# Performance work log

Measured on AMD Instinct MI355X. Metric: run time of the kernel, lower is better.

The kernel has to match this reference:

```python
import jax, jax.numpy as jnp
import numpy as np

B = 1024      # batch
M = 4096      # num_meas
W = 2         # width_per_meas
L = 2         # num_hidden_layers
Z = 64        # num_vae_latent
H = M * W     # hidden_dim = 8192


def setup_inputs() -> dict:
    key = jax.random.key(0)
    ks = jax.random.split(key, 24)

    def nrm(i, shape, scale=0.02):
        return (jax.random.normal(ks[i], shape, dtype=jnp.float32) * scale)

    return {
        "x": jax.random.normal(ks[0], (B, M), dtype=jnp.float32),
        "eps": jax.random.normal(ks[1], (B, Z), dtype=jnp.float32),
        # encoder (dense)
        "enc1_w": nrm(2, (M, M)), "enc1_b": nrm(3, (M,)),
        "enc2_w": nrm(4, (M, M)), "enc2_b": nrm(5, (M,)),
        "mu_w": nrm(6, (Z, M)), "mu_b": nrm(7, (Z,)),
        "lv_w": nrm(8, (Z, M)), "lv_b": nrm(9, (Z,)),
        # decoder mean branch: fulcon dense, hidden/output in block form
        "mean_ful_w": nrm(10, (H, Z)), "mean_ful_b": nrm(11, (H,)),
        "mean_h_w": nrm(12, (L, M, W, W)), "mean_h_b": nrm(13, (L, H)),
        "mean_out_w": nrm(14, (M, W)), "mean_out_b": nrm(15, (M,)),
        # decoder logcov branch
        "cov_ful_w": nrm(16, (H, Z)), "cov_ful_b": nrm(17, (H,)),
        "cov_h_w": nrm(18, (L, M, W, W)), "cov_h_b": nrm(19, (L, H)),
        "cov_out_w": nrm(20, (M, W)), "cov_out_b": nrm(21, (M,)),
    }


def _decoder_branch(z, ful_w, ful_b, h_w, h_b, out_w, out_b):
    # fulcon: dense latent -> hidden, then sigmoid
    a = jax.nn.sigmoid(z @ ful_w.T + ful_b)            # [B, H]
    a = a.reshape(B, M, W)                             # block-diag structure
    for l in range(L):
        # grouped block-diagonal matmul == masked dense linear of the original
        a = jax.nn.sigmoid(
            jnp.einsum('bmw,mvw->bmv', a, h_w[l]) + h_b[l].reshape(M, W)
        )
    # output mask blocks are [1, W] per measurement
    return jnp.einsum('bmw,mw->bm', a, out_w) + out_b  # [B, M]


def reference(x, eps, enc1_w, enc1_b, enc2_w, enc2_b, mu_w, mu_b, lv_w, lv_b,
              mean_ful_w, mean_ful_b, mean_h_w, mean_h_b, mean_out_w, mean_out_b,
              cov_ful_w, cov_ful_b, cov_h_w, cov_h_b, cov_out_w, cov_out_b):
    # encoder
    h = jax.nn.relu(x @ enc1_w.T + enc1_b)
    h = jax.nn.relu(h @ enc2_w.T + enc2_b)
    mu = h @ mu_w.T + mu_b
    logvar = h @ lv_w.T + lv_b
    # reparameterization (training mode, eps supplied)
    z = mu + jnp.exp(0.5 * logvar) * eps
    # decoder
    x_recon = _decoder_branch(z, mean_ful_w, mean_ful_b, mean_h_w, mean_h_b,
                              mean_out_w, mean_out_b)
    logcov = _decoder_branch(z, cov_ful_w, cov_ful_b, cov_h_w, cov_h_b,
                             cov_out_w, cov_out_b)
    return (x_recon, logcov, mu, logvar)
```

## Files before the change

### kernel.cpp

```cpp
#include <hip/hip_runtime.h>
#include <hip/hip_bf16.h>
#include <stdint.h>

typedef __hip_bfloat16 bf16;
typedef __bf16 bf16x8 __attribute__((ext_vector_type(8)));
typedef float f32x4 __attribute__((ext_vector_type(4)));

#define NB 1024
#define NM 4096
#define NZ 64
#define NH 8192

__device__ __forceinline__ float bf2f(bf16 x) { return __bfloat162float(x); }
__device__ __forceinline__ bf16 f2bf(float x) { return __float2bfloat16(x); }
__device__ __forceinline__ float sigf(float x) { return 1.f / (1.f + __expf(-x)); }

__global__ __launch_bounds__(256) void cvt_f32_bf16(const float* __restrict__ src,
                                                    bf16* __restrict__ dst, int n4) {
  const int i = blockIdx.x * 256 + threadIdx.x;
  if (i >= n4) return;
  const float4 v = ((const float4*)src)[i];
  bf16 o[4] = {f2bf(v.x), f2bf(v.y), f2bf(v.z), f2bf(v.w)};
  *(short4*)&dst[i * 4] = *(short4*)o;
}

__global__ void zero_f32(float* p, int n) {
  int i = blockIdx.x * blockDim.x + threadIdx.x;
  if (i < n) p[i] = 0.f;
}

__global__ __launch_bounds__(256) void gemm_nt(const bf16* __restrict__ A,
                                               const float* __restrict__ W,
                                               const float* __restrict__ bias,
                                               bf16* __restrict__ C,
                                               int K, int N) {
  __shared__ __attribute__((aligned(16))) bf16 smA[2][128 * 64];
  __shared__ __attribute__((aligned(16))) bf16 smB[2][64 * 64];
  const int tid  = threadIdx.x;
  const int lane = tid & 63;
  const int w    = tid >> 6;
  const int wr   = w >> 1;
  const int wc   = w & 1;

  const int lid  = blockIdx.y * 8 + blockIdx.x;
  const int wgid = (lid & 7) * 64 + (lid >> 3);
  const int row0 = (wgid & 7) * 128;
  const int col0 = (wgid >> 3) * 64;

  f32x4 acc[4][2];
#pragma unroll
  for (int i = 0; i < 4; i++)
#pragma unroll
    for (int j = 0; j < 2; j++) acc[i][j] = (f32x4){0.f, 0.f, 0.f, 0.f};

  const int swr = tid >> 2;
  const int swk = (tid & 3) * 16;
  const float* wp = W + (size_t)(col0 + swr) * K + swk;
  const int swz = (swr & 7) << 3;
  const int woff0 = swr * 64 + ((swk + 0) ^ swz);
  const int woff1 = swr * 64 + ((swk + 8) ^ swz);

  auto stage_A = [&](int buf, int kk) {
#pragma unroll
    for (int q = 0; q < 4; q++) {
      const int chunk = q * 256 + w * 64 + lane;
      const int r  = chunk >> 3;
      const int ke = ((chunk & 7) ^ (r & 7)) * 8;
      __builtin_amdgcn_global_load_lds(
          (__attribute__((address_space(1))) unsigned int*)(A + (size_t)(row0 + r) * K + (kk + ke)),
          (__attribute__((address_space(3))) unsigned int*)(&smA[buf][(q * 256 + w * 64) * 8]),
          16, 0, 0);
    }
  };

  auto write_W = [&](int buf, const float4& a, const float4& b,
                     const float4& c, const float4& d) {
    bf16 t[16] = {f2bf(a.x), f2bf(a.y), f2bf(a.z), f2bf(a.w),
                  f2bf(b.x), f2bf(b.y), f2bf(b.z), f2bf(b.w),
                  f2bf(c.x), f2bf(c.y), f2bf(c.z), f2bf(c.w),
                  f2bf(d.x), f2bf(d.y), f2bf(d.z), f2bf(d.w)};
    *(bf16x8*)&smB[buf][woff0] = ((bf16x8*)t)[0];
    *(bf16x8*)&smB[buf][woff1] = ((bf16x8*)t)[1];
  };

  auto compute = [&](int buf) {
#pragma unroll
    for (int ks = 0; ks < 64; ks += 32) {
      const int kq = ks + (lane >> 4) * 8;
      bf16x8 af[4], bfr[2];
#pragma unroll
      for (int i = 0; i < 4; i++) {
        const int r = wr * 64 + i * 16 + (lane & 15);
        af[i] = *(const bf16x8*)&smA[buf][r * 64 + (kq ^ ((r & 7) << 3))];
      }
#pragma unroll
      for (int j = 0; j < 2; j++) {
        const int r = wc * 32 + j * 16 + (lane & 15);
        bfr[j] = *(const bf16x8*)&smB[buf][r * 64 + (kq ^ ((r & 7) << 3))];
      }
#pragma unroll
      for (int i = 0; i < 4; i++)
#pragma unroll
        for (int j = 0; j < 2; j++)
          acc[i][j] = __builtin_amdgcn_mfma_f32_16x16x32_bf16(af[i], bfr[j], acc[i][j], 0, 0, 0);
    }
  };

  stage_A(0, 0);
  {
    const float4 a = *(const float4*)(wp + 0);
    const float4 b = *(const float4*)(wp + 4);
    const float4 c = *(const float4*)(wp + 8);
    const float4 d = *(const float4*)(wp + 12);
    write_W(0, a, b, c, d);
  }
  __syncthreads();

  int cur = 0;
  for (int k0 = 64; k0 < K; k0 += 64) {
    stage_A(cur ^ 1, k0);
    const float4 a = *(const float4*)(wp + k0);
    const float4 b = *(const float4*)(wp + k0 + 4);
    const float4 c = *(const float4*)(wp + k0 + 8);
    const float4 d = *(const float4*)(wp + k0 + 12);
    compute(cur);
    write_W(cur ^ 1, a, b, c, d);
    __syncthreads();
    cur ^= 1;
  }
  compute(cur);

#pragma unroll
  for (int i = 0; i < 4; i++) {
#pragma unroll
    for (int j = 0; j < 2; j++) {
      const int cc = col0 + wc * 32 + j * 16 + (lane & 15);
      const float bs = bias[cc];
#pragma unroll
      for (int t = 0; t < 4; t++) {
        const int rr = row0 + wr * 64 + i * 16 + (lane >> 4) * 4 + t;
        float v = acc[i][j][t] + bs;
        v = v > 0.f ? v : 0.f;
        C[(size_t)rr * N + cc] = f2bf(v);
      }
    }
  }
}

__global__ __launch_bounds__(256) void mulv_splitk(const bf16* __restrict__ h2,
                                                   const float* __restrict__ muw,
                                                   const float* __restrict__ lvw,
                                                   float* __restrict__ zpre) {
  __shared__ float sA[32][64];
  __shared__ float sW[32][128];
  const int tid = threadIdx.x;
  const int b0 = blockIdx.x * 64;
  const int k0 = blockIdx.y * 256;
  const int tj = tid & 15;
  const int tb = tid >> 4;
  float acc[4][8];
#pragma unroll
  for (int i = 0; i < 4; i++)
#pragma unroll
    for (int j = 0; j < 8; j++) acc[i][j] = 0.f;

  const int lb = tid >> 2, lk = (tid & 3) * 8;
  const int wj = tid >> 1, wk = (tid & 1) * 16;
  const float* wrow = (wj < 64) ? (muw + (size_t)wj * NM) : (lvw + (size_t)(wj - 64) * NM);

  for (int kc = 0; kc < 256; kc += 32) {
    __syncthreads();
    {
      const bf16* p = h2 + (size_t)(b0 + lb) * NM + (k0 + kc + lk);
#pragma unroll
      for (int i = 0; i < 8; i++) sA[lk + i][lb] = bf2f(p[i]);
      const float* q = wrow + (k0 + kc + wk);
#pragma unroll
      for (int i = 0; i < 16; i++) sW[wk + i][wj] = q[i];
    }
    __syncthreads();
#pragma unroll
    for (int k = 0; k < 32; k++) {
      float av[4], wv[8];
#pragma unroll
      for (int i = 0; i < 4; i++) av[i] = sA[k][tb * 4 + i];
#pragma unroll
      for (int j = 0; j < 8; j++) wv[j] = sW[k][tj * 8 + j];
#pragma unroll
      for (int i = 0; i < 4; i++)
#pragma unroll
        for (int j = 0; j < 8; j++) acc[i][j] += av[i] * wv[j];
    }
  }
#pragma unroll
  for (int i = 0; i < 4; i++)
#pragma unroll
    for (int j = 0; j < 8; j++)
      atomicAdd(&zpre[(size_t)(b0 + tb * 4 + i) * 128 + tj * 8 + j], acc[i][j]);
}

__global__ void zfin(const float* __restrict__ zpre, const float* __restrict__ eps,
                     const float* __restrict__ mub, const float* __restrict__ lvb,
                     float* __restrict__ out_mu, float* __restrict__ out_lv,
                     float* __restrict__ z) {
  const int i = blockIdx.x * 256 + threadIdx.x;
  const int b = i >> 6, j = i & 63;
  const float mu = zpre[(size_t)b * 128 + j] + mub[j];
  const float lv = zpre[(size_t)b * 128 + 64 + j] + lvb[j];
  const float zz = mu + expf(0.5f * lv) * eps[i];
  out_mu[i] = mu;
  out_lv[i] = lv;
  z[i] = zz;
}

__global__ __launch_bounds__(256) void dec_fused(
    const float* __restrict__ z,
    const float* __restrict__ fw, const float* __restrict__ fb,
    const float* __restrict__ hw, const float* __restrict__ hb,
    const float* __restrict__ ow, const float* __restrict__ ob,
    float* __restrict__ out) {
  __shared__ __attribute__((aligned(16))) float sZ[64][68];
  __shared__ float sFW[64][130];
  const int tid = threadIdx.x;
  const int b0 = blockIdx.x * 64;
  const int m0 = blockIdx.y * 256;
  const int mi = blockIdx.z;
  {
    const int r  = tid >> 2;
    const int c0 = (tid & 3) * 16;
    const float* p = z + (size_t)(b0 + r) * NZ + c0;
#pragma unroll
    for (int i = 0; i < 16; i++) sZ[c0 + i][r] = p[i];
  }

  const int bq = tid >> 6;
  const int tm = tid & 63;
  const int mb = m0 + mi * 64;

  {
    const int R0 = 2 * mb;
#pragma unroll
    for (int q = 0; q < 8; q++) {
      const int v = tid + q * 256;
      const int grow = v >> 4;
      const int gk = (v & 15) * 4;
      const float4 f4 = *(const float4*)&fw[(size_t)(R0 + grow) * NZ + gk];
      sFW[gk + 0][grow] = f4.x;
      sFW[gk + 1][grow] = f4.y;
      sFW[gk + 2][grow] = f4.z;
      sFW[gk + 3][grow] = f4.w;
    }
  }
  __syncthreads();

  const int m = mb + tm;
  float acc0[16], acc1[16];
  const float bb0 = fb[2 * m], bb1 = fb[2 * m + 1];
#pragma unroll
  for (int b = 0; b < 16; b++) { acc0[b] = bb0; acc1[b] = bb1; }
#pragma unroll 8
  for (int k = 0; k < 64; k++) {
    const float2 wv2 = *(const float2*)&sFW[k][2 * tm];
    const float4 z0 = *(const float4*)&sZ[k][bq * 16 + 0];
    const float4 z1 = *(const float4*)&sZ[k][bq * 16 + 4];
    const float4 z2 = *(const float4*)&sZ[k][bq * 16 + 8];
    const float4 z3 = *(const float4*)&sZ[k][bq * 16 + 12];
    const float zv[16] = {z0.x, z0.y, z0.z, z0.w, z1.x, z1.y, z1.z, z1.w,
                          z2.x, z2.y, z2.z, z2.w, z3.x, z3.y, z3.z, z3.w};
#pragma unroll
    for (int b = 0; b < 16; b++) {
      acc0[b] += zv[b] * wv2.x;
      acc1[b] += zv[b] * wv2.y;
    }
  }
  float wv[2][4], hbv[2][2];
#pragma unroll
  for (int l = 0; l < 2; l++) {
    const float4 wp = *(const float4*)&hw[((size_t)l * NM + m) * 4];
    wv[l][0] = wp.x; wv[l][1] = wp.y; wv[l][2] = wp.z; wv[l][3] = wp.w;
    const float2 hb2 = *(const float2*)&hb[(size_t)l * NH + 2 * m];
    hbv[l][0] = hb2.x; hbv[l][1] = hb2.y;
  }
  const float2 o2 = *(const float2*)&ow[2 * m];
  const float obv = ob[m];
#pragma unroll
  for (int b = 0; b < 16; b++) {
    float a0 = sigf(acc0[b]), a1 = sigf(acc1[b]);
#pragma unroll
    for (int l = 0; l < 2; l++) {
      const float v0 = sigf(wv[l][0] * a0 + wv[l][1] * a1 + hbv[l][0]);
      const float v1 = sigf(wv[l][2] * a0 + wv[l][3] * a1 + hbv[l][1]);
      a0 = v0; a1 = v1;
    }
    out[(size_t)(b0 + bq * 16 + b) * NM + m] = a0 * o2.x + a1 * o2.y + obv;
  }
}

extern "C" void kernel_launch(void* const* d_in, const int* in_sizes, int n_in,
                              void* d_out, int out_size, void* d_ws, size_t ws_size,
                              hipStream_t stream) {
  const float* x   = (const float*)d_in[0];
  const float* eps = (const float*)d_in[1];
  const float* e1w = (const float*)d_in[2];
  const float* e1b = (const float*)d_in[3];
  const float* e2w = (const float*)d_in[4];
  const float* e2b = (const float*)d_in[5];
  const float* muw = (const float*)d_in[6];
  const float* mub = (const float*)d_in[7];
  const float* lvw = (const float*)d_in[8];
  const float* lvb = (const float*)d_in[9];
  const float* mfw = (const float*)d_in[10];
  const float* mfb = (const float*)d_in[11];
  const float* mhw = (const float*)d_in[12];
  const float* mhb = (const float*)d_in[13];
  const float* mow = (const float*)d_in[14];
  const float* mob = (const float*)d_in[15];
  const float* cfw = (const float*)d_in[16];
  const float* cfb = (const float*)d_in[17];
  const float* chw = (const float*)d_in[18];
  const float* chb = (const float*)d_in[19];
  const float* cow = (const float*)d_in[20];
  const float* cob = (const float*)d_in[21];

  char* ob_ = (char*)d_out;
  float* out_x  = (float*)ob_;
  float* out_lc = (float*)(ob_ + (16u << 20));
  float* out_mu = out_x + (size_t)2 * NB * NM;
  float* out_lv = out_mu + (size_t)NB * NZ;
  bf16* h1 = (bf16*)ob_;
  bf16* xb = (bf16*)(ob_ + (16u << 20));
  bf16* h2 = xb;

  float* zpre = (float*)d_ws;
  float* z    = (float*)((char*)d_ws + (1u << 19));

  cvt_f32_bf16<<<dim3(4096), 256, 0, stream>>>(x, xb, NB * NM / 4);
  zero_f32<<<dim3(512), 256, 0, stream>>>(zpre, NB * 128);
  gemm_nt<<<dim3(8, 64), 256, 0, stream>>>(xb, e1w, e1b, h1, NM, NM);
  gemm_nt<<<dim3(8, 64), 256, 0, stream>>>(h1, e2w, e2b, h2, NM, NM);
  mulv_splitk<<<dim3(16, 16), 256, 0, stream>>>(h2, muw, lvw, zpre);
  zfin<<<dim3(256), 256, 0, stream>>>(zpre, eps, mub, lvb, out_mu, out_lv, z);
  dec_fused<<<dim3(16, 16, 4), 256, 0, stream>>>(z, mfw, mfb, mhw, mhb, mow, mob, out_x);
  dec_fused<<<dim3(16, 16, 4), 256, 0, stream>>>(z, cfw, cfb, chw, chb, cow, cob, out_lc);
}
```

Before: 524.0 us.

## Triple-buffer A tiles in encoder GEMM with explicit waitcnt pipelining; vectorize mu/logvar loads

After: 504.1 us. 1.04x faster.

```diff
diff --git a/kernel.cpp b/kernel.cpp
--- a/kernel.cpp
+++ b/kernel.cpp
@@ -29,12 +29,16 @@
   if (i < n) p[i] = 0.f;
 }
 
+#define VMW8 asm volatile("s_waitcnt vmcnt(8)" ::: "memory")
+#define VMW0 asm volatile("s_waitcnt vmcnt(0)" ::: "memory")
+#define LGKM0 asm volatile("s_waitcnt lgkmcnt(0)" ::: "memory")
+
 __global__ __launch_bounds__(256) void gemm_nt(const bf16* __restrict__ A,
                                                const float* __restrict__ W,
                                                const float* __restrict__ bias,
                                                bf16* __restrict__ C,
                                                int K, int N) {
-  __shared__ __attribute__((aligned(16))) bf16 smA[2][128 * 64];
+  __shared__ __attribute__((aligned(16))) bf16 smA[3][128 * 64];
   __shared__ __attribute__((aligned(16))) bf16 smB[2][64 * 64];
   const int tid  = threadIdx.x;
   const int lane = tid & 63;
@@ -60,7 +64,14 @@
   const int woff0 = swr * 64 + ((swk + 0) ^ swz);
   const int woff1 = swr * 64 + ((swk + 8) ^ swz);
 
-  auto stage_A = [&](int buf, int kk) {
+  auto load_W = [&](float4 (&wv)[4], int kk) {
+    wv[0] = *(const float4*)(wp + kk);
+    wv[1] = *(const float4*)(wp + kk + 4);
+    wv[2] = *(const float4*)(wp + kk + 8);
+    wv[3] = *(const float4*)(wp + kk + 12);
+  };
+
+  auto stage_A = [&](int slot, int kk) {
 #pragma unroll
     for (int q = 0; q < 4; q++) {
       const int chunk = q * 256 + w * 64 + lane;
@@ -68,22 +79,21 @@
       const int ke = ((chunk & 7) ^ (r & 7)) * 8;
       __builtin_amdgcn_global_load_lds(
           (__attribute__((address_space(1))) unsigned int*)(A + (size_t)(row0 + r) * K + (kk + ke)),
-          (__attribute__((address_space(3))) unsigned int*)(&smA[buf][(q * 256 + w * 64) * 8]),
+          (__attribute__((address_space(3))) unsigned int*)(&smA[slot][(q * 256 + w * 64) * 8]),
           16, 0, 0);
     }
   };
 
-  auto write_W = [&](int buf, const float4& a, const float4& b,
-                     const float4& c, const float4& d) {
-    bf16 t[16] = {f2bf(a.x), f2bf(a.y), f2bf(a.z), f2bf(a.w),
-                  f2bf(b.x), f2bf(b.y), f2bf(b.z), f2bf(b.w),
-                  f2bf(c.x), f2bf(c.y), f2bf(c.z), f2bf(c.w),
-                  f2bf(d.x), f2bf(d.y), f2bf(d.z), f2bf(d.w)};
-    *(bf16x8*)&smB[buf][woff0] = ((bf16x8*)t)[0];
-    *(bf16x8*)&smB[buf][woff1] = ((bf16x8*)t)[1];
+  auto write_W = [&](int slot, const float4 (&wv)[4]) {
+    bf16 t[16] = {f2bf(wv[0].x), f2bf(wv[0].y), f2bf(wv[0].z), f2bf(wv[0].w),
+                  f2bf(wv[1].x), f2bf(wv[1].y), f2bf(wv[1].z), f2bf(wv[1].w),
+                  f2bf(wv[2].x), f2bf(wv[2].y), f2bf(wv[2].z), f2bf(wv[2].w),
+                  f2bf(wv[3].x), f2bf(wv[3].y), f2bf(wv[3].z), f2bf(wv[3].w)};
+    *(bf16x8*)&smB[slot][woff0] = ((bf16x8*)t)[0];
+    *(bf16x8*)&smB[slot][woff1] = ((bf16x8*)t)[1];
   };
 
-  auto compute = [&](int buf) {
+  auto compute = [&](int sa, int ws) {
 #pragma unroll
     for (int ks = 0; ks < 64; ks += 32) {
       const int kq = ks + (lane >> 4) * 8;
@@ -91,12 +101,12 @@
 #pragma unroll
       for (int i = 0; i < 4; i++) {
         const int r = wr * 64 + i * 16 + (lane & 15);
-        af[i] = *(const bf16x8*)&smA[buf][r * 64 + (kq ^ ((r & 7) << 3))];
+        af[i] = *(const bf16x8*)&smA[sa][r * 64 + (kq ^ ((r & 7) << 3))];
       }
 #pragma unroll
       for (int j = 0; j < 2; j++) {
         const int r = wc * 32 + j * 16 + (lane & 15);
-        bfr[j] = *(const bf16x8*)&smB[buf][r * 64 + (kq ^ ((r & 7) << 3))];
+        bfr[j] = *(const bf16x8*)&smB[ws][r * 64 + (kq ^ ((r & 7) << 3))];
       }
 #pragma unroll
       for (int i = 0; i < 4; i++)
@@ -106,29 +116,49 @@
     }
   };
 
+  const int K64 = K >> 6;
+  float4 wA[4], wB[4];
+
+  load_W(wA, 0);
   stage_A(0, 0);
-  {
-    const float4 a = *(const float4*)(wp + 0);
-    const float4 b = *(const float4*)(wp + 4);
-    const float4 c = *(const float4*)(wp + 8);
-    const float4 d = *(const float4*)(wp + 12);
-    write_W(0, a, b, c, d);
-  }
-  __syncthreads();
-
-  int cur = 0;
-  for (int k0 = 64; k0 < K; k0 += 64) {
-    stage_A(cur ^ 1, k0);
-    const float4 a = *(const float4*)(wp + k0);
-    const float4 b = *(const float4*)(wp + k0 + 4);
-    const float4 c = *(const float4*)(wp + k0 + 8);
-    const float4 d = *(const float4*)(wp + k0 + 12);
-    compute(cur);
-    write_W(cur ^ 1, a, b, c, d);
-    __syncthreads();
-    cur ^= 1;
-  }
-  compute(cur);
+  asm volatile("" ::: "memory");
+  load_W(wB, 64);
+  stage_A(1, 64);
+
+  int sa = 0;
+  for (int i = 0; i + 2 < K64; i += 2) {
+    const int nx  = (sa + 1 == 3) ? 0 : sa + 1;
+    const int nnx = (nx + 1 == 3) ? 0 : nx + 1;
+    VMW8;
+    write_W(0, wA);
+    LGKM0;
+    __builtin_amdgcn_s_barrier();
+    __builtin_amdgcn_sched_barrier(0);
+    load_W(wA, (i + 2) * 64);
+    stage_A(nnx, (i + 2) * 64);
+    compute(sa, 0);
+    VMW8;
+    write_W(1, wB);
+    LGKM0;
+    __builtin_amdgcn_s_barrier();
+    __builtin_amdgcn_sched_barrier(0);
+    load_W(wB, (i + 3) * 64);
+    stage_A(sa, (i + 3) * 64);
+    compute(nx, 1);
+    sa = nnx;
+  }
+  VMW8;
+  write_W(0, wA);
+  LGKM0;
+  __builtin_amdgcn_s_barrier();
+  __builtin_amdgcn_sched_barrier(0);
+  compute(sa, 0);
+  VMW0;
+  write_W(1, wB);
+  LGKM0;
+  __builtin_amdgcn_s_barrier();
+  __builtin_amdgcn_sched_barrier(0);
+  compute((sa + 1 == 3) ? 0 : sa + 1, 1);
 
 #pragma unroll
   for (int i = 0; i < 4; i++) {
@@ -171,12 +201,24 @@
   for (int kc = 0; kc < 256; kc += 32) {
     __syncthreads();
     {
-      const bf16* p = h2 + (size_t)(b0 + lb) * NM + (k0 + kc + lk);
-#pragma unroll
-      for (int i = 0; i < 8; i++) sA[lk + i][lb] = bf2f(p[i]);
+      const uint4 v = *(const uint4*)(h2 + (size_t)(b0 + lb) * NM + (k0 + kc + lk));
+      sA[lk + 0][lb] = __uint_as_float(v.x << 16);
+      sA[lk + 1][lb] = __uint_as_float(v.x & 0xffff0000u);
+      sA[lk + 2][lb] = __uint_as_float(v.y << 16);
+      sA[lk + 3][lb] = __uint_as_float(v.y & 0xffff0000u);
+      sA[lk + 4][lb] = __uint_as_float(v.z << 16);
+      sA[lk + 5][lb] = __uint_as_float(v.z & 0xffff0000u);
+      sA[lk + 6][lb] = __uint_as_float(v.w << 16);
+      sA[lk + 7][lb] = __uint_as_float(v.w & 0xffff0000u);
       const float* q = wrow + (k0 + kc + wk);
 #pragma unroll
-      for (int i = 0; i < 16; i++) sW[wk + i][wj] = q[i];
+      for (int i = 0; i < 4; i++) {
+        const float4 f = *(const float4*)(q + i * 4);
+        sW[wk + i * 4 + 0][wj] = f.x;
+        sW[wk + i * 4 + 1][wj] = f.y;
+        sW[wk + i * 4 + 2][wj] = f.z;
+        sW[wk + i * 4 + 3][wj] = f.w;
+      }
     }
     __syncthreads();
 #pragma unroll
```
